# Kernel tuning notes

Hardware: AMD Instinct MI355X
Metric: run time of the kernel (lower is better)

## Reference

```python
import jax, jax.numpy as jnp
import numpy as np

B, S, D, H = 2, 4096, 512, 8
DH = D // H
EPS = 1e-5


def setup_inputs() -> dict:
    key = jax.random.key(0)
    ks = jax.random.split(key, 8)
    s = 0.02
    return {
        "x": jax.random.normal(ks[0], (B, S, D), jnp.float32),
        "in_proj_w": jax.random.normal(ks[1], (3 * D, D), jnp.float32) * s,
        "in_proj_b": jnp.zeros((3 * D,), jnp.float32),
        "out_proj_w": jax.random.normal(ks[2], (D, D), jnp.float32) * s,
        "out_proj_b": jnp.zeros((D,), jnp.float32),
        "ln1_g": jnp.ones((D,), jnp.float32),
        "ln1_b": jnp.zeros((D,), jnp.float32),
        "ln2_g": jnp.ones((D,), jnp.float32),
        "ln2_b": jnp.zeros((D,), jnp.float32),
        "w1": jax.random.normal(ks[3], (D, D), jnp.float32) * s,
        "b1": jnp.zeros((D,), jnp.float32),
        "w2": jax.random.normal(ks[4], (D, D), jnp.float32) * s,
        "b2": jnp.zeros((D,), jnp.float32),
        "window": 256,
    }


def _layernorm(x, g, b):
    mu = jnp.mean(x, axis=-1, keepdims=True)
    var = jnp.mean(jnp.square(x - mu), axis=-1, keepdims=True)
    return (x - mu) * jax.lax.rsqrt(var + EPS) * g + b


def reference(x, in_proj_w, in_proj_b, out_proj_w, out_proj_b,
              ln1_g, ln1_b, ln2_g, ln2_b, w1, b1, w2, b2, window):
    b, s, d = x.shape
    # sliding-window mask: allowed iff |i - j| <= window
    idx = jnp.arange(s)
    allowed = jnp.abs(idx[:, None] - idx[None, :]) <= window  # [S,S]

    # fused QKV projection (torch MultiheadAttention layout: W [3D, D])
    qkv = x @ in_proj_w.T + in_proj_b  # [B,S,3D]
    q, k, v = jnp.split(qkv, 3, axis=-1)
    q = q.reshape(b, s, H, DH)
    k = k.reshape(b, s, H, DH)
    v = v.reshape(b, s, H, DH)

    scale = 1.0 / jnp.sqrt(jnp.float32(DH))
    scores = jnp.einsum("bqhd,bkhd->bhqk", q, k) * scale  # [B,H,S,S]
    scores = jnp.where(allowed[None, None], scores, -jnp.inf)
    attn = jax.nn.softmax(scores, axis=-1)
    ctx = jnp.einsum("bhqk,bkhd->bqhd", attn, v).reshape(b, s, d)
    attn_out = ctx @ out_proj_w.T + out_proj_b

    # residual + LayerNorm (dropout rate 0 -> identity)
    h = _layernorm(x + attn_out, ln1_g, ln1_b)
    mlp = jax.nn.relu(h @ w1.T + b1) @ w2.T + b2
    return _layernorm(h + mlp, ln2_g, ln2_b)
```

## Files before the change

kernel.cpp:

```cpp
#include <hip/hip_runtime.h>

typedef __bf16 bf16;
typedef __bf16 bf16x2 __attribute__((ext_vector_type(2)));
typedef __bf16 bf16x8 __attribute__((ext_vector_type(8)));
typedef float f32x4 __attribute__((ext_vector_type(4)));

#define S_LEN 4096
#define DMODEL 512
#define NHEAD 8
#define DHEAD 64
#define BATCH 2
#define M_ROWS (BATCH * S_LEN)
#define K_DIM 512
#define QKV_LD 1536

__device__ __forceinline__ void async16(void* lds, const void* g) {
  __builtin_amdgcn_global_load_lds(
      (const __attribute__((address_space(1))) unsigned int*)g,
      (__attribute__((address_space(3))) unsigned int*)lds, 16, 0, 0);
}

__global__ void detect_dtype(const unsigned int* __restrict__ x,
                             int* __restrict__ flag) {
  const int lane = threadIdx.x;
  int cnt = 0;
#pragma unroll
  for (int i = 0; i < 16; ++i) {
    const unsigned int w = x[lane * 16 + i];
    const unsigned int e = (w >> 7) & 0xFFu;
    cnt += (e >= 100u && e <= 140u) ? 1 : 0;
  }
#pragma unroll
  for (int off = 1; off < 64; off <<= 1) cnt += __shfl_xor(cnt, off);
  if (lane == 0) *flag = (cnt >= 700) ? 1 : 0;
}

__device__ __forceinline__ bf16x8 ld8(const void* p, size_t e, bool asF32) {
  if (asF32) {
    const float* q = (const float*)p + e;
    const float4 a = *(const float4*)q;
    const float4 b = *(const float4*)(q + 4);
    bf16x8 r;
    r[0] = (bf16)a.x; r[1] = (bf16)a.y; r[2] = (bf16)a.z; r[3] = (bf16)a.w;
    r[4] = (bf16)b.x; r[5] = (bf16)b.y; r[6] = (bf16)b.z; r[7] = (bf16)b.w;
    return r;
  }
  return *(const bf16x8*)((const bf16*)p + e);
}

__device__ __forceinline__ float ld1(const void* p, size_t e, bool asF32) {
  return asF32 ? ((const float*)p)[e] : (float)((const bf16*)p)[e];
}

__global__ __launch_bounds__(256) void cvt_weights(const void* __restrict__ s0,
                                                   const void* __restrict__ s1,
                                                   const void* __restrict__ s2,
                                                   const void* __restrict__ s3,
                                                   bf16* __restrict__ dst,
                                                   const int* __restrict__ flag) {
  const bool f32in = (*flag == 0);
  const int b = blockIdx.x;
  const void* s;
  size_t doff;
  int lb;
  if (b < 384)      { s = s0; doff = 0;        lb = b; }
  else if (b < 512) { s = s1; doff = 786432;   lb = b - 384; }
  else if (b < 640) { s = s2; doff = 1048576;  lb = b - 512; }
  else              { s = s3; doff = 1310720;  lb = b - 640; }
  const size_t idx = (size_t)lb * 2048 + threadIdx.x * 8;
  *(bf16x8*)(dst + doff + idx) = ld8(s, idx, f32in);
}

__global__ __launch_bounds__(256) void cvt_x(const void* __restrict__ x,
                                             bf16* __restrict__ xb,
                                             const int* __restrict__ flag) {
  const bool f32in = (*flag == 0);
  const size_t idx = ((size_t)blockIdx.x * 256 + threadIdx.x) * 8;
  *(bf16x8*)(xb + idx) = ld8(x, idx, f32in);
}

template <int BN, bool RELU>
__global__ __launch_bounds__(256) void gemm_bt(const bf16* __restrict__ A,
                                               const bf16* __restrict__ W,
                                               const void* __restrict__ bias,
                                               bf16* __restrict__ C, int N,
                                               const int* __restrict__ flag) {
  __shared__ __align__(16) bf16 As[128 * 64];
  __shared__ __align__(16) bf16 Ws[BN * 64];

  const bool f32in = (*flag == 0);

  const int t = threadIdx.x;
  const int lane = t & 63;
  const int wave = t >> 6;
  constexpr int MT = (BN == 128) ? 4 : 2;
  const int wm = (BN == 128) ? (wave >> 1) * 64 : wave * 32;
  const int wn = (BN == 128) ? (wave & 1) * 64 : 0;
  const int l16 = lane & 15;
  const int quad = lane >> 4;
  const int m0 = blockIdx.y * 128;
  const int n0 = blockIdx.x * BN;

  const int rr = lane >> 3;
  const int cb = (lane & 7) ^ rr;
  const int sw = l16 & 7;

  f32x4 acc[MT][4];
#pragma unroll
  for (int i = 0; i < MT; ++i)
#pragma unroll
    for (int j = 0; j < 4; ++j) acc[i][j] = (f32x4){0.f, 0.f, 0.f, 0.f};

  for (int kt = 0; kt < K_DIM; kt += 64) {
    __syncthreads();
#pragma unroll
    for (int i = 0; i < 4; ++i) {
      const int r0 = wave * 32 + i * 8;
      async16(&As[r0 * 64], &A[(size_t)(m0 + r0 + rr) * K_DIM + kt + cb * 8]);
    }
#pragma unroll
    for (int i = 0; i < BN / 32; ++i) {
      const int r0 = wave * (BN / 4) + i * 8;
      async16(&Ws[r0 * 64], &W[(size_t)(n0 + r0 + rr) * K_DIM + kt + cb * 8]);
    }
    __syncthreads();
#pragma unroll
    for (int ks = 0; ks < 2; ++ks) {
      bf16x8 af[MT], wf[4];
#pragma unroll
      for (int mt = 0; mt < MT; ++mt)
        af[mt] = *(const bf16x8*)&As[(wm + mt * 16 + l16) * 64 +
                                     (((ks * 4 + quad) ^ sw) * 8)];
#pragma unroll
      for (int nt = 0; nt < 4; ++nt)
        wf[nt] = *(const bf16x8*)&Ws[(wn + nt * 16 + l16) * 64 +
                                     (((ks * 4 + quad) ^ sw) * 8)];
#pragma unroll
      for (int mt = 0; mt < MT; ++mt)
#pragma unroll
        for (int nt = 0; nt < 4; ++nt)
          acc[mt][nt] = __builtin_amdgcn_mfma_f32_16x16x32_bf16(af[mt], wf[nt],
                                                                acc[mt][nt], 0, 0, 0);
    }
  }

#pragma unroll
  for (int nt = 0; nt < 4; ++nt) {
    const int n = n0 + wn + nt * 16 + l16;
    const float bv = ld1(bias, n, f32in);
#pragma unroll
    for (int mt = 0; mt < MT; ++mt) {
#pragma unroll
      for (int r = 0; r < 4; ++r) {
        const int m = m0 + wm + mt * 16 + quad * 4 + r;
        float v = acc[mt][nt][r] + bv;
        if (RELU) v = fmaxf(v, 0.f);
        C[(size_t)m * N + n] = (bf16)v;
      }
    }
  }
}

__global__ __launch_bounds__(256) void attn_fwd(const bf16* __restrict__ qkv,
                                                bf16* __restrict__ ctx,
                                                const int* __restrict__ wptr) {
  __shared__ __align__(16) bf16 Vt[2][64][72];
  __shared__ __align__(16) bf16 Pbuf[4][16][72];

  const int t = threadIdx.x;
  const int lane = t & 63;
  const int wave = t >> 6;
  const int l16 = lane & 15;
  const int quad = lane >> 4;

  const int nqb = S_LEN / 64;
  const int qblk = blockIdx.x % nqb;
  const int h = (blockIdx.x / nqb) % NHEAD;
  const int b = blockIdx.x / (nqb * NHEAD);
  const int qbase = qblk * 64;
  int window = *wptr;
  if (window < 0) window = 0;
  if (window > S_LEN) window = S_LEN;
  const float scale = 0.125f;

  const int qrow = qbase + wave * 16 + l16;
  const bf16* qp = qkv + (size_t)(b * S_LEN + qrow) * QKV_LD + h * DHEAD;
  const bf16x8 qf0 = *(const bf16x8*)(qp + quad * 8);
  const bf16x8 qf1 = *(const bf16x8*)(qp + 32 + quad * 8);

  f32x4 o[4];
#pragma unroll
  for (int nt = 0; nt < 4; ++nt) o[nt] = (f32x4){0.f, 0.f, 0.f, 0.f};
  float lp[4] = {0.f, 0.f, 0.f, 0.f};

  int kstart = qbase - window;
  if (kstart < 0) kstart = 0;
  kstart &= ~63;
  int kend = qbase + 64 + window;
  if (kend > S_LEN) kend = S_LEN;
  const int niter = (kend - kstart + 63) >> 6;

  const int vk = (t & 31) * 2;
  const int vd = (t >> 5) * 8;
  const bf16* vbase = qkv + (size_t)(b * S_LEN) * QKV_LD + 2 * DMODEL + h * DHEAD + vd;
  const bf16* kbase = qkv + (size_t)(b * S_LEN) * QKV_LD + DMODEL + h * DHEAD;

  {
    const bf16* p = vbase + (size_t)(kstart + vk) * QKV_LD;
    const bf16x8 va = *(const bf16x8*)p;
    const bf16x8 vb = *(const bf16x8*)(p + QKV_LD);
#pragma unroll
    for (int j = 0; j < 8; ++j) {
      bf16x2 pr; pr[0] = va[j]; pr[1] = vb[j];
      *(bf16x2*)&Vt[0][vd + j][vk] = pr;
    }
  }

  for (int it = 0; it < niter; ++it) {
    const int kt = kstart + it * 64;
    const int cur = it & 1;
    __syncthreads();

    bf16x8 na, nb;
    const bool have_next = (it + 1 < niter);
    if (have_next) {
      const bf16* p = vbase + (size_t)(kt + 64 + vk) * QKV_LD;
      na = *(const bf16x8*)p;
      nb = *(const bf16x8*)(p + QKV_LD);
    }

    f32x4 s[4];
#pragma unroll
    for (int t4 = 0; t4 < 4; ++t4) s[t4] = (f32x4){0.f, 0.f, 0.f, 0.f};
#pragma unroll
    for (int t4 = 0; t4 < 4; ++t4) {
      const bf16* kp = kbase + (size_t)(kt + t4 * 16 + l16) * QKV_LD;
      const bf16x8 k0 = *(const bf16x8*)(kp + quad * 8);
      const bf16x8 k1 = *(const bf16x8*)(kp + 32 + quad * 8);
      s[t4] = __builtin_amdgcn_mfma_f32_16x16x32_bf16(qf0, k0, s[t4], 0, 0, 0);
      s[t4] = __builtin_amdgcn_mfma_f32_16x16x32_bf16(qf1, k1, s[t4], 0, 0, 0);
    }

#pragma unroll
    for (int r = 0; r < 4; ++r) {
      const int q = qbase + wave * 16 + quad * 4 + r;
      float psum = 0.f;
#pragma unroll
      for (int t4 = 0; t4 < 4; ++t4) {
        const int key = kt + t4 * 16 + l16;
        int d = q - key; if (d < 0) d = -d;
        const float p = (d <= window) ? __expf(s[t4][r] * scale) : 0.f;
        psum += p;
        Pbuf[wave][quad * 4 + r][t4 * 16 + l16] = (bf16)p;
      }
      lp[r] += psum;
    }

    const bf16x8 pf0 = *(const bf16x8*)&Pbuf[wave][l16][quad * 8];
    const bf16x8 pf1 = *(const bf16x8*)&Pbuf[wave][l16][32 + quad * 8];
#pragma unroll
    for (int nt = 0; nt < 4; ++nt) {
      const bf16x8 v0 = *(const bf16x8*)&Vt[cur][nt * 16 + l16][quad * 8];
      const bf16x8 v1 = *(const bf16x8*)&Vt[cur][nt * 16 + l16][32 + quad * 8];
      o[nt] = __builtin_amdgcn_mfma_f32_16x16x32_bf16(pf0, v0, o[nt], 0, 0, 0);
      o[nt] = __builtin_amdgcn_mfma_f32_16x16x32_bf16(pf1, v1, o[nt], 0, 0, 0);
    }

    if (have_next) {
#pragma unroll
      for (int j = 0; j < 8; ++j) {
        bf16x2 pr; pr[0] = na[j]; pr[1] = nb[j];
        *(bf16x2*)&Vt[cur ^ 1][vd + j][vk] = pr;
      }
    }
  }

#pragma unroll
  for (int r = 0; r < 4; ++r) {
#pragma unroll
    for (int off = 1; off < 16; off <<= 1) lp[r] += __shfl_xor(lp[r], off);
    const float inv = (lp[r] > 0.f) ? (1.0f / lp[r]) : 0.f;
    const int q = qbase + wave * 16 + quad * 4 + r;
#pragma unroll
    for (int nt = 0; nt < 4; ++nt) {
      ctx[(size_t)(b * S_LEN + q) * DMODEL + h * DHEAD + nt * 16 + l16] =
          (bf16)(o[nt][r] * inv);
    }
  }
}

template <bool A_RAW, bool OUT_RAW>
__global__ __launch_bounds__(256) void ln_fused(const void* __restrict__ a,
                                                const bf16* __restrict__ bres,
                                                const void* __restrict__ g,
                                                const void* __restrict__ be,
                                                void* __restrict__ out,
                                                const int* __restrict__ flag) {
  const bool f32in = (*flag == 0);
  const int row = blockIdx.x * 4 + (threadIdx.x >> 6);
  const int lane = threadIdx.x & 63;
  const size_t base = (size_t)row * DMODEL + lane * 8;
  const bf16x8 va = ld8(a, base, A_RAW && f32in);
  const bf16x8 vb = *(const bf16x8*)(bres + base);
  float v[8], s = 0.f, s2 = 0.f;
#pragma unroll
  for (int j = 0; j < 8; ++j) {
    v[j] = (float)va[j] + (float)vb[j];
    s += v[j];
    s2 += v[j] * v[j];
  }
#pragma unroll
  for (int off = 1; off < 64; off <<= 1) {
    s += __shfl_xor(s, off);
    s2 += __shfl_xor(s2, off);
  }
  const float mean = s * (1.0f / DMODEL);
  float var = s2 * (1.0f / DMODEL) - mean * mean;
  if (var < 0.f) var = 0.f;
  const float rstd = rsqrtf(var + 1e-5f);
  const bf16x8 gv = ld8(g, lane * 8, f32in);
  const bf16x8 bev = ld8(be, lane * 8, f32in);
  float ov[8];
#pragma unroll
  for (int j = 0; j < 8; ++j)
    ov[j] = (v[j] - mean) * rstd * (float)gv[j] + (float)bev[j];
  if (OUT_RAW && f32in) {
    float4 o0 = {ov[0], ov[1], ov[2], ov[3]};
    float4 o1 = {ov[4], ov[5], ov[6], ov[7]};
    *(float4*)((float*)out + base) = o0;
    *(float4*)((float*)out + base + 4) = o1;
  } else {
    bf16x8 ob;
#pragma unroll
    for (int j = 0; j < 8; ++j) ob[j] = (bf16)ov[j];
    *(bf16x8*)((bf16*)out + base) = ob;
  }
}

extern "C" void kernel_launch(void* const* d_in, const int* in_sizes, int n_in,
                              void* d_out, int out_size, void* d_ws, size_t ws_size,
                              hipStream_t stream) {
  const void* x          = d_in[0];
  const void* in_proj_w  = d_in[1];
  const void* in_proj_b  = d_in[2];
  const void* out_proj_w = d_in[3];
  const void* out_proj_b = d_in[4];
  const void* ln1_g      = d_in[5];
  const void* ln1_b      = d_in[6];
  const void* ln2_g      = d_in[7];
  const void* ln2_b      = d_in[8];
  const void* w1         = d_in[9];
  const void* b1         = d_in[10];
  const void* w2         = d_in[11];
  const void* b2         = d_in[12];
  const int*  wptr       = (const int*)d_in[13];

  char* ws = (char*)d_ws;
  int* flag = (int*)ws;
  bf16* warena = (bf16*)(ws + 256);
  bf16* wq = warena;
  bf16* wo = warena + 786432;
  bf16* w1b = warena + 1048576;
  bf16* w2b = warena + 1310720;
  char* big = ws + 256 + 3145728;
  bf16* qkv      = (bf16*)big;
  bf16* h        = (bf16*)big;
  bf16* a1       = (bf16*)(big + 8388608);
  bf16* attn_out = (bf16*)(big + 16777216);
  bf16* mlp      = attn_out;
  bf16* xb       = (bf16*)d_out;
  bf16* ctx      = (bf16*)d_out;

  detect_dtype<<<1, 64, 0, stream>>>((const unsigned int*)x, flag);
  cvt_weights<<<768, 256, 0, stream>>>(in_proj_w, out_proj_w, w1, w2, warena, flag);
  cvt_x<<<2048, 256, 0, stream>>>(x, xb, flag);
  gemm_bt<128, false><<<dim3(QKV_LD / 128, M_ROWS / 128), 256, 0, stream>>>(
      xb, wq, in_proj_b, qkv, QKV_LD, flag);
  attn_fwd<<<dim3(BATCH * NHEAD * (S_LEN / 64)), 256, 0, stream>>>(qkv, ctx, wptr);
  gemm_bt<64, false><<<dim3(DMODEL / 64, M_ROWS / 128), 256, 0, stream>>>(
      ctx, wo, out_proj_b, attn_out, DMODEL, flag);
  ln_fused<true, false><<<dim3(M_ROWS / 4), 256, 0, stream>>>(
      x, attn_out, ln1_g, ln1_b, h, flag);
  gemm_bt<64, true><<<dim3(DMODEL / 64, M_ROWS / 128), 256, 0, stream>>>(
      h, w1b, b1, a1, DMODEL, flag);
  gemm_bt<64, false><<<dim3(DMODEL / 64, M_ROWS / 128), 256, 0, stream>>>(
      a1, w2b, b2, mlp, DMODEL, flag);
  ln_fused<false, true><<<dim3(M_ROWS / 4), 256, 0, stream>>>(
      h, mlp, ln2_g, ln2_b, d_out, flag);
}
```

Baseline: 230.5 us.

## Use double-buffered 64x64 GEMM tiles, merge conversion kernels, remap attention blocks to XCDs

```diff
diff --git a/kernel.cpp b/kernel.cpp
--- a/kernel.cpp
+++ b/kernel.cpp
@@ -13,12 +13,6 @@
 #define M_ROWS (BATCH * S_LEN)
 #define K_DIM 512
 #define QKV_LD 1536
-
-__device__ __forceinline__ void async16(void* lds, const void* g) {
-  __builtin_amdgcn_global_load_lds(
-      (const __attribute__((address_space(1))) unsigned int*)g,
-      (__attribute__((address_space(3))) unsigned int*)lds, 16, 0, 0);
-}
 
 __global__ void detect_dtype(const unsigned int* __restrict__ x,
                              int* __restrict__ flag) {
@@ -52,104 +46,123 @@
   return asF32 ? ((const float*)p)[e] : (float)((const bf16*)p)[e];
 }
 
-__global__ __launch_bounds__(256) void cvt_weights(const void* __restrict__ s0,
-                                                   const void* __restrict__ s1,
-                                                   const void* __restrict__ s2,
-                                                   const void* __restrict__ s3,
-                                                   bf16* __restrict__ dst,
-                                                   const int* __restrict__ flag) {
+__global__ __launch_bounds__(256) void cvt_all(const void* __restrict__ x,
+                                               const void* __restrict__ s0,
+                                               const void* __restrict__ s1,
+                                               const void* __restrict__ s2,
+                                               const void* __restrict__ s3,
+                                               bf16* __restrict__ xb,
+                                               bf16* __restrict__ warena,
+                                               const int* __restrict__ flag) {
   const bool f32in = (*flag == 0);
   const int b = blockIdx.x;
+  if (b < 2048) {
+    const size_t idx = ((size_t)b * 256 + threadIdx.x) * 8;
+    *(bf16x8*)(xb + idx) = ld8(x, idx, f32in);
+    return;
+  }
+  const int wb = b - 2048;
   const void* s;
   size_t doff;
   int lb;
-  if (b < 384)      { s = s0; doff = 0;        lb = b; }
-  else if (b < 512) { s = s1; doff = 786432;   lb = b - 384; }
-  else if (b < 640) { s = s2; doff = 1048576;  lb = b - 512; }
-  else              { s = s3; doff = 1310720;  lb = b - 640; }
+  if (wb < 384)      { s = s0; doff = 0;        lb = wb; }
+  else if (wb < 512) { s = s1; doff = 786432;   lb = wb - 384; }
+  else if (wb < 640) { s = s2; doff = 1048576;  lb = wb - 512; }
+  else               { s = s3; doff = 1310720;  lb = wb - 640; }
   const size_t idx = (size_t)lb * 2048 + threadIdx.x * 8;
-  *(bf16x8*)(dst + doff + idx) = ld8(s, idx, f32in);
-}
-
-__global__ __launch_bounds__(256) void cvt_x(const void* __restrict__ x,
-                                             bf16* __restrict__ xb,
-                                             const int* __restrict__ flag) {
-  const bool f32in = (*flag == 0);
-  const size_t idx = ((size_t)blockIdx.x * 256 + threadIdx.x) * 8;
-  *(bf16x8*)(xb + idx) = ld8(x, idx, f32in);
-}
-
-template <int BN, bool RELU>
-__global__ __launch_bounds__(256) void gemm_bt(const bf16* __restrict__ A,
-                                               const bf16* __restrict__ W,
-                                               const void* __restrict__ bias,
-                                               bf16* __restrict__ C, int N,
-                                               const int* __restrict__ flag) {
-  __shared__ __align__(16) bf16 As[128 * 64];
-  __shared__ __align__(16) bf16 Ws[BN * 64];
+  *(bf16x8*)(warena + doff + idx) = ld8(s, idx, f32in);
+}
+
+template <bool RELU>
+__global__ __launch_bounds__(256) void gemm64(const bf16* __restrict__ A,
+                                              const bf16* __restrict__ W,
+                                              const void* __restrict__ bias,
+                                              bf16* __restrict__ C, int N,
+                                              const int* __restrict__ flag) {
+  __shared__ __align__(16) bf16 As[2][64 * 64];
+  __shared__ __align__(16) bf16 Ws[2][64 * 64];
 
   const bool f32in = (*flag == 0);
 
   const int t = threadIdx.x;
   const int lane = t & 63;
   const int wave = t >> 6;
-  constexpr int MT = (BN == 128) ? 4 : 2;
-  const int wm = (BN == 128) ? (wave >> 1) * 64 : wave * 32;
-  const int wn = (BN == 128) ? (wave & 1) * 64 : 0;
   const int l16 = lane & 15;
   const int quad = lane >> 4;
-  const int m0 = blockIdx.y * 128;
-  const int n0 = blockIdx.x * BN;
+  const int m0 = blockIdx.y * 64;
+  const int n0 = blockIdx.x * 64;
+  const int wm = (wave >> 1) * 32;
+  const int wn = (wave & 1) * 32;
 
   const int rr = lane >> 3;
   const int cb = (lane & 7) ^ rr;
   const int sw = l16 & 7;
-
-  f32x4 acc[MT][4];
-#pragma unroll
-  for (int i = 0; i < MT; ++i)
-#pragma unroll
-    for (int j = 0; j < 4; ++j) acc[i][j] = (f32x4){0.f, 0.f, 0.f, 0.f};
-
-  for (int kt = 0; kt < K_DIM; kt += 64) {
+  const int arow = wave * 16 + rr;
+  const int lslot = (wave * 16 + rr) * 64 + (lane & 7) * 8;
+
+  f32x4 acc[2][2];
+#pragma unroll
+  for (int i = 0; i < 2; ++i)
+#pragma unroll
+    for (int j = 0; j < 2; ++j) acc[i][j] = (f32x4){0.f, 0.f, 0.f, 0.f};
+
+  uint4 ra[2], rw[2];
+#pragma unroll
+  for (int i = 0; i < 2; ++i) {
+    ra[i] = *(const uint4*)&A[(size_t)(m0 + arow + i * 8) * K_DIM + cb * 8];
+    rw[i] = *(const uint4*)&W[(size_t)(n0 + arow + i * 8) * K_DIM + cb * 8];
+  }
+#pragma unroll
+  for (int i = 0; i < 2; ++i) {
+    *(uint4*)&As[0][lslot + i * 8 * 64] = ra[i];
+    *(uint4*)&Ws[0][lslot + i * 8 * 64] = rw[i];
+  }
+
+  for (int it = 0; it < K_DIM / 64; ++it) {
+    const int cur = it & 1;
+    const bool have_next = (it + 1 < K_DIM / 64);
+    if (have_next) {
+      const int kt = (it + 1) * 64;
+#pragma unroll
+      for (int i = 0; i < 2; ++i) {
+        ra[i] = *(const uint4*)&A[(size_t)(m0 + arow + i * 8) * K_DIM + kt + cb * 8];
+        rw[i] = *(const uint4*)&W[(size_t)(n0 + arow + i * 8) * K_DIM + kt + cb * 8];
+      }
+    }
     __syncthreads();
 #pragma unroll
-    for (int i = 0; i < 4; ++i) {
-      const int r0 = wave * 32 + i * 8;
-      async16(&As[r0 * 64], &A[(size_t)(m0 + r0 + rr) * K_DIM + kt + cb * 8]);
-    }
-#pragma unroll
-    for (int i = 0; i < BN / 32; ++i) {
-      const int r0 = wave * (BN / 4) + i * 8;
-      async16(&Ws[r0 * 64], &W[(size_t)(n0 + r0 + rr) * K_DIM + kt + cb * 8]);
-    }
-    __syncthreads();
-#pragma unroll
     for (int ks = 0; ks < 2; ++ks) {
-      bf16x8 af[MT], wf[4];
-#pragma unroll
-      for (int mt = 0; mt < MT; ++mt)
-        af[mt] = *(const bf16x8*)&As[(wm + mt * 16 + l16) * 64 +
-                                     (((ks * 4 + quad) ^ sw) * 8)];
-#pragma unroll
-      for (int nt = 0; nt < 4; ++nt)
-        wf[nt] = *(const bf16x8*)&Ws[(wn + nt * 16 + l16) * 64 +
-                                     (((ks * 4 + quad) ^ sw) * 8)];
-#pragma unroll
-      for (int mt = 0; mt < MT; ++mt)
-#pragma unroll
-        for (int nt = 0; nt < 4; ++nt)
+      bf16x8 af[2], wf[2];
+#pragma unroll
+      for (int mt = 0; mt < 2; ++mt)
+        af[mt] = *(const bf16x8*)&As[cur][(wm + mt * 16 + l16) * 64 +
+                                          (((ks * 4 + quad) ^ sw) * 8)];
+#pragma unroll
+      for (int nt = 0; nt < 2; ++nt)
+        wf[nt] = *(const bf16x8*)&Ws[cur][(wn + nt * 16 + l16) * 64 +
+                                          (((ks * 4 + quad) ^ sw) * 8)];
+#pragma unroll
+      for (int mt = 0; mt < 2; ++mt)
+#pragma unroll
+        for (int nt = 0; nt < 2; ++nt)
           acc[mt][nt] = __builtin_amdgcn_mfma_f32_16x16x32_bf16(af[mt], wf[nt],
                                                                 acc[mt][nt], 0, 0, 0);
     }
-  }
-
-#pragma unroll
-  for (int nt = 0; nt < 4; ++nt) {
+    if (have_next) {
+#pragma unroll
+      for (int i = 0; i < 2; ++i) {
+        *(uint4*)&As[cur ^ 1][lslot + i * 8 * 64] = ra[i];
+        *(uint4*)&Ws[cur ^ 1][lslot + i * 8 * 64] = rw[i];
+      }
+    }
+  }
+
+#pragma unroll
+  for (int nt = 0; nt < 2; ++nt) {
     const int n = n0 + wn + nt * 16 + l16;
     const float bv = ld1(bias, n, f32in);
 #pragma unroll
-    for (int mt = 0; mt < MT; ++mt) {
+    for (int mt = 0; mt < 2; ++mt) {
 #pragma unroll
       for (int r = 0; r < 4; ++r) {
         const int m = m0 + wm + mt * 16 + quad * 4 + r;
@@ -173,10 +186,13 @@
   const int l16 = lane & 15;
   const int quad = lane >> 4;
 
-  const int nqb = S_LEN / 64;
-  const int qblk = blockIdx.x % nqb;
-  const int h = (blockIdx.x / nqb) % NHEAD;
-  const int b = blockIdx.x / (nqb * NHEAD);
+  const int bid = blockIdx.x;
+  const int xcd = bid & 7;
+  const int jj = bid >> 3;
+  const int pair = xcd * 2 + (jj >> 6);
+  const int qblk = jj & 63;
+  const int h = pair & 7;
+  const int b = pair >> 3;
   const int qbase = qblk * 64;
   int window = *wptr;
   if (window < 0) window = 0;
@@ -244,12 +260,12 @@
 #pragma unroll
     for (int r = 0; r < 4; ++r) {
       const int q = qbase + wave * 16 + quad * 4 + r;
+      const int lo = q - window, hi = q + window;
       float psum = 0.f;
 #pragma unroll
       for (int t4 = 0; t4 < 4; ++t4) {
         const int key = kt + t4 * 16 + l16;
-        int d = q - key; if (d < 0) d = -d;
-        const float p = (d <= window) ? __expf(s[t4][r] * scale) : 0.f;
+        const float p = (key >= lo && key <= hi) ? __expf(s[t4][r] * scale) : 0.f;
         psum += p;
         Pbuf[wave][quad * 4 + r][t4 * 16 + l16] = (bf16)p;
       }
@@ -372,18 +388,17 @@
   bf16* ctx      = (bf16*)d_out;
 
   detect_dtype<<<1, 64, 0, stream>>>((const unsigned int*)x, flag);
-  cvt_weights<<<768, 256, 0, stream>>>(in_proj_w, out_proj_w, w1, w2, warena, flag);
-  cvt_x<<<2048, 256, 0, stream>>>(x, xb, flag);
-  gemm_bt<128, false><<<dim3(QKV_LD / 128, M_ROWS / 128), 256, 0, stream>>>(
+  cvt_all<<<2816, 256, 0, stream>>>(x, in_proj_w, out_proj_w, w1, w2, xb, warena, flag);
+  gemm64<false><<<dim3(QKV_LD / 64, M_ROWS / 64), 256, 0, stream>>>(
       xb, wq, in_proj_b, qkv, QKV_LD, flag);
   attn_fwd<<<dim3(BATCH * NHEAD * (S_LEN / 64)), 256, 0, stream>>>(qkv, ctx, wptr);
-  gemm_bt<64, false><<<dim3(DMODEL / 64, M_ROWS / 128), 256, 0, stream>>>(
+  gemm64<false><<<dim3(DMODEL / 64, M_ROWS / 64), 256, 0, stream>>>(
       ctx, wo, out_proj_b, attn_out, DMODEL, flag);
   ln_fused<true, false><<<dim3(M_ROWS / 4), 256, 0, stream>>>(
       x, attn_out, ln1_g, ln1_b, h, flag);
-  gemm_bt<64, true><<<dim3(DMODEL / 64, M_ROWS / 128), 256, 0, stream>>>(
+  gemm64<true><<<dim3(DMODEL / 64, M_ROWS / 64), 256, 0, stream>>>(
       h, w1b, b1, a1, DMODEL, flag);
-  gemm_bt<64, false><<<dim3(DMODEL / 64, M_ROWS / 128), 256, 0, stream>>>(
+  gemm64<false><<<dim3(DMODEL / 64, M_ROWS / 64), 256, 0, stream>>>(
       a1, w2b, b2, mlp, DMODEL, flag);
   ln_fused<false, true><<<dim3(M_ROWS / 4), 256, 0, stream>>>(
       h, mlp, ln2_g, ln2_b, d_out, flag);
```

Measured after the change: 358.7 us. +55.6%, slower.
